# Performance work log

Measured on AMD Instinct MI355X. Metric: run time of the kernel, lower is better.

The kernel has to match this reference:

```python
import jax, jax.numpy as jnp
import numpy as np

B, T, F = 8, 512, 256
G, V = 2, 8192          # num_codebooks, num_embeddings per group
D = 16
DG = D // G             # per-group codevector dim = 8


def setup_inputs() -> dict:
    key = jax.random.key(0)
    k1, k2, k3, k4, k5 = jax.random.split(key, 5)
    x = jax.random.normal(k1, (B, T, F), dtype=jnp.float32)
    u = jax.random.uniform(k2, (B * T * G, V), dtype=jnp.float32)  # uniform for gumbel
    input_mask = jnp.ones((B, T), dtype=jnp.int32)
    embeddings = jax.random.uniform(k3, (1, G * V, DG), dtype=jnp.float32)
    W_proj = jax.random.normal(k4, (G * V, F), dtype=jnp.float32) * 0.02
    b_proj = jnp.zeros((G * V,), dtype=jnp.float32)
    return {"x": x, "u": u, "embeddings": embeddings,
            "W_proj": W_proj, "b_proj": b_proj, "input_mask": input_mask}


def reference(x, u, embeddings, W_proj, b_proj, input_mask):
    temperature = 1.0
    b, t, _ = x.shape
    # weight projection: [b, t, G*V]
    hidden = jnp.einsum("btf,gf->btg", x, W_proj) + b_proj
    h = hidden.reshape(b * t * G, V)
    # gumbel noise from uniform sample (matches torch.empty().uniform_(tiny, 1))
    tiny = jnp.finfo(h.dtype).tiny
    gumbels = -jnp.log(-jnp.log(jnp.clip(u, tiny, 1.0)))
    codevector_probs = jax.nn.softmax((h + gumbels) / temperature, axis=-1)  # [btG, V]
    # soft distribution (no noise) for perplexity
    soft = jax.nn.softmax(h.reshape(b * t, G, V), axis=-1)
    mask = input_mask.reshape(-1).astype(bool)  # [bt]
    masked = jnp.where(mask[:, None, None], soft, 0.0)
    marginal = masked.sum(0) / input_mask.sum().astype(soft.dtype)  # [G, V]
    perplexity = jnp.exp(-jnp.sum(marginal * jnp.log(marginal + 1e-7), axis=-1)).sum()
    targets_idx = jnp.argmax(codevector_probs, axis=-1).reshape(b, t, G)
    # per-group weighted codebook combination as GEMM (no huge broadcast intermediate)
    pg = codevector_probs.reshape(b * t, G, V)
    emb = embeddings.reshape(G, V, DG)
    codevectors = jnp.einsum("ngv,gvd->ngd", pg, emb).reshape(b, t, G * DG)
    return (codevectors, perplexity, targets_idx)
```

## Files before the change

### kernel.cpp

```cpp
#include <hip/hip_runtime.h>
#include <hip/hip_bf16.h>
#include <math.h>

#define Mrows 4096
#define Kdim  256
#define Ncols 16384
#define Vsz   8192

typedef __attribute__((ext_vector_type(8))) short bf16x8;
typedef __attribute__((ext_vector_type(4))) float f32x4;

__global__ __launch_bounds__(256) void split_bf16(const float* __restrict__ src,
                                                  __hip_bfloat16* __restrict__ hi,
                                                  __hip_bfloat16* __restrict__ lo) {
    const int i = blockIdx.x * 256 + threadIdx.x;
    const float v = src[i];
    const __hip_bfloat16 h = __float2bfloat16(v);
    const float hf = __bfloat162float(h);
    hi[i] = h;
    lo[i] = __float2bfloat16(v - hf);
}

__global__ __launch_bounds__(256) void gemm_mfma(const __hip_bfloat16* __restrict__ Ahi,
                                                 const __hip_bfloat16* __restrict__ Alo,
                                                 const __hip_bfloat16* __restrict__ Bhi,
                                                 const __hip_bfloat16* __restrict__ Blo,
                                                 const float* __restrict__ bias,
                                                 float* __restrict__ hid, int r0) {
    __shared__ unsigned short Ah[128 * 32], Al[128 * 32], Bh[128 * 32], Bl[128 * 32];
    const int tid = threadIdx.x;
    const int lane = tid & 63;
    const int wave = tid >> 6;
    const int bm = blockIdx.x * 128;
    const int bn = blockIdx.y * 128;
    const int wm = (wave & 1) * 64;
    const int wn = (wave >> 1) * 64;
    const int lm = lane & 15;
    const int kq = (lane >> 4) * 8;

    f32x4 acc[4][4];
#pragma unroll
    for (int i = 0; i < 4; ++i)
#pragma unroll
        for (int j = 0; j < 4; ++j) acc[i][j] = (f32x4){0.f, 0.f, 0.f, 0.f};

    for (int k0 = 0; k0 < Kdim; k0 += 32) {
        __syncthreads();
#pragma unroll
        for (int t = 0; t < 2; ++t) {
            const int c = tid + t * 256;
            const int row = c >> 2;
            const int ko = (c & 3) * 8;
            const size_t ga = (size_t)(r0 + bm + row) * Kdim + k0 + ko;
            const size_t gb = (size_t)(bn + row) * Kdim + k0 + ko;
            *(uint4*)&Ah[row * 32 + ko] = *(const uint4*)(Ahi + ga);
            *(uint4*)&Al[row * 32 + ko] = *(const uint4*)(Alo + ga);
            *(uint4*)&Bh[row * 32 + ko] = *(const uint4*)(Bhi + gb);
            *(uint4*)&Bl[row * 32 + ko] = *(const uint4*)(Blo + gb);
        }
        __syncthreads();

        bf16x8 ah[4], al[4], bh[4], bl[4];
#pragma unroll
        for (int i = 0; i < 4; ++i) {
            ah[i] = *(const bf16x8*)&Ah[(wm + i * 16 + lm) * 32 + kq];
            al[i] = *(const bf16x8*)&Al[(wm + i * 16 + lm) * 32 + kq];
            bh[i] = *(const bf16x8*)&Bh[(wn + i * 16 + lm) * 32 + kq];
            bl[i] = *(const bf16x8*)&Bl[(wn + i * 16 + lm) * 32 + kq];
        }
#pragma unroll
        for (int i = 0; i < 4; ++i)
#pragma unroll
            for (int j = 0; j < 4; ++j) {
                acc[i][j] = __builtin_amdgcn_mfma_f32_16x16x32_bf16(ah[i], bh[j], acc[i][j], 0, 0, 0);
                acc[i][j] = __builtin_amdgcn_mfma_f32_16x16x32_bf16(ah[i], bl[j], acc[i][j], 0, 0, 0);
                acc[i][j] = __builtin_amdgcn_mfma_f32_16x16x32_bf16(al[i], bh[j], acc[i][j], 0, 0, 0);
            }
    }

    const int rbase = (lane >> 4) * 4;
#pragma unroll
    for (int j = 0; j < 4; ++j) {
        const int n = bn + wn + j * 16 + lm;
        const float bj = bias[n];
#pragma unroll
        for (int i = 0; i < 4; ++i) {
            const int m0 = bm + wm + i * 16 + rbase;
#pragma unroll
            for (int r2 = 0; r2 < 4; ++r2)
                hid[(size_t)(m0 + r2) * Ncols + n] = acc[i][j][r2] + bj;
        }
    }
}

__global__ __launch_bounds__(256) void phase2(const float* __restrict__ hid,
                                              const float* __restrict__ u,
                                              const float* __restrict__ emb,
                                              const int* __restrict__ mask,
                                              float* __restrict__ marginal,
                                              float* __restrict__ out,
                                              int r0) {
    const int g = blockIdx.y;
    const int n0 = r0 + blockIdx.x * 8;
    const int tid = threadIdx.x;
    const int lane = tid & 63;
    const int wid = tid >> 6;

    __shared__ float marg_s[32 * 256];
    __shared__ float sv1[4]; __shared__ int si1[4]; __shared__ float sv2[4];
    __shared__ float ss1[4], ss2[4], scv[4][8];

#pragma unroll
    for (int i = 0; i < 32; ++i) marg_s[(i << 8) + tid] = 0.f;

    const float* embg = emb + (size_t)g * Vsz * 8;
    float lg[32];

    for (int r = 0; r < 8; ++r) {
        const int n = n0 + r;
        const float* hrow = hid + (size_t)(n - r0) * Ncols + (size_t)g * Vsz;
        const float* urow = u + ((size_t)n * 2 + g) * Vsz;

        float mx1 = -INFINITY, mx2 = -INFINITY;
        int amax = 0;
#pragma unroll
        for (int i = 0; i < 32; ++i) {
            const int v = (i << 8) + tid;
            const float hv = hrow[v];
            float uu = urow[v];
            uu = fminf(fmaxf(uu, 1.17549435e-38f), 1.0f);
            const float d = uu - 1.0f;
            float q = 1.0f / 9.0f;
            q = fmaf(q, d, -0.125f);
            q = fmaf(q, d, 1.0f / 7.0f);
            q = fmaf(q, d, -1.0f / 6.0f);
            q = fmaf(q, d, 0.2f);
            q = fmaf(q, d, -0.25f);
            q = fmaf(q, d, 1.0f / 3.0f);
            q = fmaf(q, d, -0.5f);
            q = fmaf(q, d, 1.0f);
            const float inner = (d > -0.2f) ? (-d) * q : -__logf(uu);
            const float l = hv - __logf(inner);
            lg[i] = l;
            if (l > mx1) { mx1 = l; amax = v; }
            mx2 = fmaxf(mx2, hv);
        }
        float v1 = mx1; int i1 = amax; float v2 = mx2;
#pragma unroll
        for (int off = 32; off > 0; off >>= 1) {
            const float ov = __shfl_down(v1, off);
            const int oi = __shfl_down(i1, off);
            if (ov > v1 || (ov == v1 && oi < i1)) { v1 = ov; i1 = oi; }
            v2 = fmaxf(v2, __shfl_down(v2, off));
        }
        if (lane == 0) { sv1[wid] = v1; si1[wid] = i1; sv2[wid] = v2; }
        __syncthreads();
        if (tid == 0) {
            float bv = sv1[0]; int bi = si1[0]; float b2 = sv2[0];
            for (int w2 = 1; w2 < 4; ++w2) {
                if (sv1[w2] > bv || (sv1[w2] == bv && si1[w2] < bi)) { bv = sv1[w2]; bi = si1[w2]; }
                b2 = fmaxf(b2, sv2[w2]);
            }
            sv1[0] = bv; si1[0] = bi; sv2[0] = b2;
        }
        __syncthreads();
        const float M1 = sv1[0];
        const float M2 = sv2[0];
        const int AMAX = si1[0];

        float s1 = 0.f, s2 = 0.f;
        float cv[8];
#pragma unroll
        for (int d2 = 0; d2 < 8; ++d2) cv[d2] = 0.f;
#pragma unroll
        for (int i = 0; i < 32; ++i) {
            const int v = (i << 8) + tid;
            const float p = __expf(lg[i] - M1);
            s1 += p;
            const float4 e0 = *(const float4*)(embg + (size_t)v * 8);
            const float4 e1 = *(const float4*)(embg + (size_t)v * 8 + 4);
            cv[0] = fmaf(p, e0.x, cv[0]); cv[1] = fmaf(p, e0.y, cv[1]);
            cv[2] = fmaf(p, e0.z, cv[2]); cv[3] = fmaf(p, e0.w, cv[3]);
            cv[4] = fmaf(p, e1.x, cv[4]); cv[5] = fmaf(p, e1.y, cv[5]);
            cv[6] = fmaf(p, e1.z, cv[6]); cv[7] = fmaf(p, e1.w, cv[7]);
            const float qq = __expf(hrow[v] - M2);
            s2 += qq;
            lg[i] = qq;
        }
#pragma unroll
        for (int off = 32; off > 0; off >>= 1) {
            s1 += __shfl_down(s1, off);
            s2 += __shfl_down(s2, off);
        }
#pragma unroll
        for (int d2 = 0; d2 < 8; ++d2)
#pragma unroll
            for (int off = 32; off > 0; off >>= 1) cv[d2] += __shfl_down(cv[d2], off);
        if (lane == 0) {
            ss1[wid] = s1; ss2[wid] = s2;
#pragma unroll
            for (int d2 = 0; d2 < 8; ++d2) scv[wid][d2] = cv[d2];
        }
        __syncthreads();
        if (tid == 0) {
            ss1[0] = ss1[0] + ss1[1] + ss1[2] + ss1[3];
            ss2[0] = ss2[0] + ss2[1] + ss2[2] + ss2[3];
        }
        __syncthreads();
        const float S1 = ss1[0];
        const float S2 = ss2[0];
        if (tid < 8) {
            const float c = scv[0][tid] + scv[1][tid] + scv[2][tid] + scv[3][tid];
            out[(size_t)n * 16 + g * 8 + tid] = c / S1;
        }
        if (tid == 8) out[65537 + (size_t)n * 2 + g] = (float)AMAX;

        if (mask[n] != 0) {
            const float invS2 = 1.0f / S2;
#pragma unroll
            for (int i = 0; i < 32; ++i)
                marg_s[(i << 8) + tid] = fmaf(lg[i], invS2, marg_s[(i << 8) + tid]);
        }
        __syncthreads();
    }
#pragma unroll
    for (int i = 0; i < 32; ++i)
        atomicAdd(&marginal[g * Vsz + (i << 8) + tid], marg_s[(i << 8) + tid]);
}

__global__ __launch_bounds__(256) void ppl_kernel(const float* __restrict__ marginal,
                                                  const int* __restrict__ mask,
                                                  float* __restrict__ out) {
    const int tid = threadIdx.x;
    const int lane = tid & 63;
    const int wid = tid >> 6;
    __shared__ float red[4];
    __shared__ int redi[4];

    int ms = 0;
    for (int i = tid; i < Mrows; i += 256) ms += mask[i];
#pragma unroll
    for (int off = 32; off > 0; off >>= 1) ms += __shfl_down(ms, off);
    if (lane == 0) redi[wid] = ms;
    __syncthreads();
    const float inv = 1.0f / (float)(redi[0] + redi[1] + redi[2] + redi[3]);

    float ppl = 0.f;
    for (int g = 0; g < 2; ++g) {
        float part = 0.f;
        for (int v = tid; v < Vsz; v += 256) {
            const float m = marginal[g * Vsz + v] * inv;
            part += m * logf(m + 1e-7f);
        }
#pragma unroll
        for (int off = 32; off > 0; off >>= 1) part += __shfl_down(part, off);
        __syncthreads();
        if (lane == 0) red[wid] = part;
        __syncthreads();
        if (tid == 0) ppl += __expf(-(red[0] + red[1] + red[2] + red[3]));
        __syncthreads();
    }
    if (tid == 0) out[65536] = ppl;
}

extern "C" void kernel_launch(void* const* d_in, const int* in_sizes, int n_in,
                              void* d_out, int out_size, void* d_ws, size_t ws_size,
                              hipStream_t stream) {
    const float* x    = (const float*)d_in[0];
    const float* u    = (const float*)d_in[1];
    const float* emb  = (const float*)d_in[2];
    const float* w    = (const float*)d_in[3];
    const float* bias = (const float*)d_in[4];
    const int*   mask = (const int*)d_in[5];
    float* out = (float*)d_out;

    char* base = (char*)d_ws;
    float* marginal = (float*)base;
    __hip_bfloat16* Ahi = (__hip_bfloat16*)(base + 65536);
    __hip_bfloat16* Alo = Ahi + 1048576;
    __hip_bfloat16* Bhi = Alo + 1048576;
    __hip_bfloat16* Blo = Bhi + 4194304;
    const size_t hid_off = 65536 + 4194304 + 16777216;
    float* hid = (float*)(base + hid_off);

    size_t cap_rows = (ws_size > hid_off) ? (ws_size - hid_off) / ((size_t)Ncols * 4) : 0;
    int cr = (cap_rows >= Mrows) ? Mrows : (int)((cap_rows / 128) * 128);
    if (cr < 128) cr = 128;

    hipMemsetAsync(marginal, 0, 65536, stream);
    split_bf16<<<4096, 256, 0, stream>>>(x, Ahi, Alo);
    split_bf16<<<16384, 256, 0, stream>>>(w, Bhi, Blo);

    for (int r0 = 0; r0 < Mrows; r0 += cr) {
        const int rows = (Mrows - r0 < cr) ? (Mrows - r0) : cr;
        dim3 gg(rows / 128, Ncols / 128);
        gemm_mfma<<<gg, 256, 0, stream>>>(Ahi, Alo, Bhi, Blo, bias, hid, r0);
        dim3 pg(rows / 8, 2);
        phase2<<<pg, 256, 0, stream>>>(hid, u, emb, mask, marginal, out, r0);
    }
    ppl_kernel<<<1, 256, 0, stream>>>(marginal, mask, out);
}
```

Before: 896.1 us.

## Use direct global-to-LDS loads in GEMM and widen phase2 to 512 threads

The GEMM tile loads now use global_load_lds, so data goes straight into shared memory instead of passing through registers first. In phase2 the block grows to 512 threads, each handling 16 elements per row through float4 vector loads of hid and u rather than 32 scalar loads. The trailing per-row __syncthreads is removed, and the marginal atomics are remapped to the new layout. Risks: the LDS layout in the GEMM must still match the c*8 indexing, and removing the barrier relies on each thread owning its own marg_s entries.

New measurement: 887.5 us. No clear change (-1.0%).

```diff
diff --git a/kernel.cpp b/kernel.cpp
--- a/kernel.cpp
+++ b/kernel.cpp
@@ -9,6 +9,10 @@
 
 typedef __attribute__((ext_vector_type(8))) short bf16x8;
 typedef __attribute__((ext_vector_type(4))) float f32x4;
+
+#define GLD16(ldsp, gp) __builtin_amdgcn_global_load_lds(                          \
+    (const __attribute__((address_space(1))) unsigned int*)(gp),                   \
+    (__attribute__((address_space(3))) unsigned int*)(ldsp), 16, 0, 0)
 
 __global__ __launch_bounds__(256) void split_bf16(const float* __restrict__ src,
                                                   __hip_bfloat16* __restrict__ hi,
@@ -53,10 +57,10 @@
             const int ko = (c & 3) * 8;
             const size_t ga = (size_t)(r0 + bm + row) * Kdim + k0 + ko;
             const size_t gb = (size_t)(bn + row) * Kdim + k0 + ko;
-            *(uint4*)&Ah[row * 32 + ko] = *(const uint4*)(Ahi + ga);
-            *(uint4*)&Al[row * 32 + ko] = *(const uint4*)(Alo + ga);
-            *(uint4*)&Bh[row * 32 + ko] = *(const uint4*)(Bhi + gb);
-            *(uint4*)&Bl[row * 32 + ko] = *(const uint4*)(Blo + gb);
+            GLD16(&Ah[c * 8], Ahi + ga);
+            GLD16(&Al[c * 8], Alo + ga);
+            GLD16(&Bh[c * 8], Bhi + gb);
+            GLD16(&Bl[c * 8], Blo + gb);
         }
         __syncthreads();
 
@@ -93,28 +97,28 @@
     }
 }
 
-__global__ __launch_bounds__(256) void phase2(const float* __restrict__ hid,
-                                              const float* __restrict__ u,
-                                              const float* __restrict__ emb,
-                                              const int* __restrict__ mask,
-                                              float* __restrict__ marginal,
-                                              float* __restrict__ out,
-                                              int r0) {
+__global__ __launch_bounds__(512, 4) void phase2(const float* __restrict__ hid,
+                                                 const float* __restrict__ u,
+                                                 const float* __restrict__ emb,
+                                                 const int* __restrict__ mask,
+                                                 float* __restrict__ marginal,
+                                                 float* __restrict__ out,
+                                                 int r0) {
     const int g = blockIdx.y;
     const int n0 = r0 + blockIdx.x * 8;
     const int tid = threadIdx.x;
     const int lane = tid & 63;
     const int wid = tid >> 6;
 
-    __shared__ float marg_s[32 * 256];
-    __shared__ float sv1[4]; __shared__ int si1[4]; __shared__ float sv2[4];
-    __shared__ float ss1[4], ss2[4], scv[4][8];
-
-#pragma unroll
-    for (int i = 0; i < 32; ++i) marg_s[(i << 8) + tid] = 0.f;
+    __shared__ float marg_s[16 * 512];
+    __shared__ float sv1[8]; __shared__ int si1[8]; __shared__ float sv2[8];
+    __shared__ float ss1[8], ss2[8], scv[8][8];
+
+#pragma unroll
+    for (int k = 0; k < 16; ++k) marg_s[(k << 9) + tid] = 0.f;
 
     const float* embg = emb + (size_t)g * Vsz * 8;
-    float lg[32];
+    float lg[16];
 
     for (int r = 0; r < 8; ++r) {
         const int n = n0 + r;
@@ -124,40 +128,45 @@
         float mx1 = -INFINITY, mx2 = -INFINITY;
         int amax = 0;
 #pragma unroll
-        for (int i = 0; i < 32; ++i) {
-            const int v = (i << 8) + tid;
-            const float hv = hrow[v];
-            float uu = urow[v];
-            uu = fminf(fmaxf(uu, 1.17549435e-38f), 1.0f);
-            const float d = uu - 1.0f;
-            float q = 1.0f / 9.0f;
-            q = fmaf(q, d, -0.125f);
-            q = fmaf(q, d, 1.0f / 7.0f);
-            q = fmaf(q, d, -1.0f / 6.0f);
-            q = fmaf(q, d, 0.2f);
-            q = fmaf(q, d, -0.25f);
-            q = fmaf(q, d, 1.0f / 3.0f);
-            q = fmaf(q, d, -0.5f);
-            q = fmaf(q, d, 1.0f);
-            const float inner = (d > -0.2f) ? (-d) * q : -__logf(uu);
-            const float l = hv - __logf(inner);
-            lg[i] = l;
-            if (l > mx1) { mx1 = l; amax = v; }
-            mx2 = fmaxf(mx2, hv);
-        }
-        float v1 = mx1; int i1 = amax; float v2 = mx2;
+        for (int i = 0; i < 4; ++i) {
+            const int vb = (i << 11) + (tid << 2);
+            const float4 hv4 = *(const float4*)(hrow + vb);
+            const float4 uu4 = *(const float4*)(urow + vb);
+#define GUM(j, hv, uraw) {                                                        \
+            float uu = fminf(fmaxf((uraw), 1.17549435e-38f), 1.0f);               \
+            const float d = uu - 1.0f;                                            \
+            float q = 1.0f / 9.0f;                                                \
+            q = fmaf(q, d, -0.125f);                                              \
+            q = fmaf(q, d, 1.0f / 7.0f);                                          \
+            q = fmaf(q, d, -1.0f / 6.0f);                                         \
+            q = fmaf(q, d, 0.2f);                                                 \
+            q = fmaf(q, d, -0.25f);                                               \
+            q = fmaf(q, d, 1.0f / 3.0f);                                          \
+            q = fmaf(q, d, -0.5f);                                                \
+            q = fmaf(q, d, 1.0f);                                                 \
+            const float inner = (d > -0.2f) ? (-d) * q : -__logf(uu);             \
+            const float l = (hv) - __logf(inner);                                 \
+            lg[(i << 2) + (j)] = l;                                               \
+            if (l > mx1) { mx1 = l; amax = vb + (j); }                            \
+            mx2 = fmaxf(mx2, (hv)); }
+            GUM(0, hv4.x, uu4.x)
+            GUM(1, hv4.y, uu4.y)
+            GUM(2, hv4.z, uu4.z)
+            GUM(3, hv4.w, uu4.w)
+#undef GUM
+        }
 #pragma unroll
         for (int off = 32; off > 0; off >>= 1) {
-            const float ov = __shfl_down(v1, off);
-            const int oi = __shfl_down(i1, off);
-            if (ov > v1 || (ov == v1 && oi < i1)) { v1 = ov; i1 = oi; }
-            v2 = fmaxf(v2, __shfl_down(v2, off));
-        }
-        if (lane == 0) { sv1[wid] = v1; si1[wid] = i1; sv2[wid] = v2; }
+            const float ov = __shfl_down(mx1, off);
+            const int oi = __shfl_down(amax, off);
+            if (ov > mx1 || (ov == mx1 && oi < amax)) { mx1 = ov; amax = oi; }
+            mx2 = fmaxf(mx2, __shfl_down(mx2, off));
+        }
+        if (lane == 0) { sv1[wid] = mx1; si1[wid] = amax; sv2[wid] = mx2; }
         __syncthreads();
         if (tid == 0) {
             float bv = sv1[0]; int bi = si1[0]; float b2 = sv2[0];
-            for (int w2 = 1; w2 < 4; ++w2) {
+            for (int w2 = 1; w2 < 8; ++w2) {
                 if (sv1[w2] > bv || (sv1[w2] == bv && si1[w2] < bi)) { bv = sv1[w2]; bi = si1[w2]; }
                 b2 = fmaxf(b2, sv2[w2]);
             }
@@ -173,19 +182,26 @@
 #pragma unroll
         for (int d2 = 0; d2 < 8; ++d2) cv[d2] = 0.f;
 #pragma unroll
-        for (int i = 0; i < 32; ++i) {
-            const int v = (i << 8) + tid;
-            const float p = __expf(lg[i] - M1);
-            s1 += p;
-            const float4 e0 = *(const float4*)(embg + (size_t)v * 8);
-            const float4 e1 = *(const float4*)(embg + (size_t)v * 8 + 4);
-            cv[0] = fmaf(p, e0.x, cv[0]); cv[1] = fmaf(p, e0.y, cv[1]);
-            cv[2] = fmaf(p, e0.z, cv[2]); cv[3] = fmaf(p, e0.w, cv[3]);
-            cv[4] = fmaf(p, e1.x, cv[4]); cv[5] = fmaf(p, e1.y, cv[5]);
-            cv[6] = fmaf(p, e1.z, cv[6]); cv[7] = fmaf(p, e1.w, cv[7]);
-            const float qq = __expf(hrow[v] - M2);
-            s2 += qq;
-            lg[i] = qq;
+        for (int i = 0; i < 4; ++i) {
+            const int vb = (i << 11) + (tid << 2);
+            const float4 hv4 = *(const float4*)(hrow + vb);
+#define PB(j, hv) {                                                               \
+            const float p = __expf(lg[(i << 2) + (j)] - M1);                      \
+            s1 += p;                                                              \
+            const float4 e0 = *(const float4*)(embg + (size_t)(vb + (j)) * 8);    \
+            const float4 e1 = *(const float4*)(embg + (size_t)(vb + (j)) * 8 + 4);\
+            cv[0] = fmaf(p, e0.x, cv[0]); cv[1] = fmaf(p, e0.y, cv[1]);           \
+            cv[2] = fmaf(p, e0.z, cv[2]); cv[3] = fmaf(p, e0.w, cv[3]);           \
+            cv[4] = fmaf(p, e1.x, cv[4]); cv[5] = fmaf(p, e1.y, cv[5]);           \
+            cv[6] = fmaf(p, e1.z, cv[6]); cv[7] = fmaf(p, e1.w, cv[7]);           \
+            const float qq = __expf((hv) - M2);                                   \
+            s2 += qq;                                                             \
+            lg[(i << 2) + (j)] = qq; }
+            PB(0, hv4.x)
+            PB(1, hv4.y)
+            PB(2, hv4.z)
+            PB(3, hv4.w)
+#undef PB
         }
 #pragma unroll
         for (int off = 32; off > 0; off >>= 1) {
@@ -203,14 +219,17 @@
         }
         __syncthreads();
         if (tid == 0) {
-            ss1[0] = ss1[0] + ss1[1] + ss1[2] + ss1[3];
-            ss2[0] = ss2[0] + ss2[1] + ss2[2] + ss2[3];
+            float a = 0.f, b = 0.f;
+            for (int w2 = 0; w2 < 8; ++w2) { a += ss1[w2]; b += ss2[w2]; }
+            ss1[0] = a; ss2[0] = b;
         }
         __syncthreads();
         const float S1 = ss1[0];
         const float S2 = ss2[0];
         if (tid < 8) {
-            const float c = scv[0][tid] + scv[1][tid] + scv[2][tid] + scv[3][tid];
+            float c = 0.f;
+#pragma unroll
+            for (int w2 = 0; w2 < 8; ++w2) c += scv[w2][tid];
             out[(size_t)n * 16 + g * 8 + tid] = c / S1;
         }
         if (tid == 8) out[65537 + (size_t)n * 2 + g] = (float)AMAX;
@@ -218,14 +237,14 @@
         if (mask[n] != 0) {
             const float invS2 = 1.0f / S2;
 #pragma unroll
-            for (int i = 0; i < 32; ++i)
-                marg_s[(i << 8) + tid] = fmaf(lg[i], invS2, marg_s[(i << 8) + tid]);
-        }
-        __syncthreads();
-    }
-#pragma unroll
-    for (int i = 0; i < 32; ++i)
-        atomicAdd(&marginal[g * Vsz + (i << 8) + tid], marg_s[(i << 8) + tid]);
+            for (int k = 0; k < 16; ++k)
+                marg_s[(k << 9) + tid] = fmaf(lg[k], invS2, marg_s[(k << 9) + tid]);
+        }
+    }
+#pragma unroll
+    for (int k = 0; k < 16; ++k)
+        atomicAdd(&marginal[g * Vsz + ((k >> 2) << 11) + (tid << 2) + (k & 3)],
+                  marg_s[(k << 9) + tid]);
 }
 
 __global__ __launch_bounds__(256) void ppl_kernel(const float* __restrict__ marginal,
@@ -296,7 +315,7 @@
         dim3 gg(rows / 128, Ncols / 128);
         gemm_mfma<<<gg, 256, 0, stream>>>(Ahi, Alo, Bhi, Blo, bias, hid, r0);
         dim3 pg(rows / 8, 2);
-        phase2<<<pg, 256, 0, stream>>>(hid, u, emb, mask, marginal, out, r0);
+        phase2<<<pg, 512, 0, stream>>>(hid, u, emb, mask, marginal, out, r0);
     }
     ppl_kernel<<<1, 256, 0, stream>>>(marginal, mask, out);
 }
```

## Use direct global-to-LDS loads in GEMM and register-resident marginals in phase2

Applied to the files above, without the earlier changes.

The GEMM now fills LDS with global_load_lds 16-byte transfers instead of staging through registers. It loads B fragments per column inside the MFMA loop and requests 3 blocks per CU. Phase2 moves to 512-thread blocks, keeps the marginal accumulators and hidden values in registers instead of a 32KB LDS array, and drops a re-read of hid. The row chunk size is capped at 2048 so the hidden buffer stays smaller and more cache-friendly, at the cost of one extra launch pair.

Result: slower. 1.010 ms (+12.8%).

```diff
diff --git a/kernel.cpp b/kernel.cpp
--- a/kernel.cpp
+++ b/kernel.cpp
@@ -9,6 +9,10 @@
 
 typedef __attribute__((ext_vector_type(8))) short bf16x8;
 typedef __attribute__((ext_vector_type(4))) float f32x4;
+
+#define GLD16(ldsp, gp) __builtin_amdgcn_global_load_lds(                          \
+    (const __attribute__((address_space(1))) unsigned int*)(gp),                   \
+    (__attribute__((address_space(3))) unsigned int*)(ldsp), 16, 0, 0)
 
 __global__ __launch_bounds__(256) void split_bf16(const float* __restrict__ src,
                                                   __hip_bfloat16* __restrict__ hi,
@@ -21,12 +25,12 @@
     lo[i] = __float2bfloat16(v - hf);
 }
 
-__global__ __launch_bounds__(256) void gemm_mfma(const __hip_bfloat16* __restrict__ Ahi,
-                                                 const __hip_bfloat16* __restrict__ Alo,
-                                                 const __hip_bfloat16* __restrict__ Bhi,
-                                                 const __hip_bfloat16* __restrict__ Blo,
-                                                 const float* __restrict__ bias,
-                                                 float* __restrict__ hid, int r0) {
+__global__ __launch_bounds__(256, 3) void gemm_mfma(const __hip_bfloat16* __restrict__ Ahi,
+                                                    const __hip_bfloat16* __restrict__ Alo,
+                                                    const __hip_bfloat16* __restrict__ Bhi,
+                                                    const __hip_bfloat16* __restrict__ Blo,
+                                                    const float* __restrict__ bias,
+                                                    float* __restrict__ hid, int r0) {
     __shared__ unsigned short Ah[128 * 32], Al[128 * 32], Bh[128 * 32], Bl[128 * 32];
     const int tid = threadIdx.x;
     const int lane = tid & 63;
@@ -53,29 +57,30 @@
             const int ko = (c & 3) * 8;
             const size_t ga = (size_t)(r0 + bm + row) * Kdim + k0 + ko;
             const size_t gb = (size_t)(bn + row) * Kdim + k0 + ko;
-            *(uint4*)&Ah[row * 32 + ko] = *(const uint4*)(Ahi + ga);
-            *(uint4*)&Al[row * 32 + ko] = *(const uint4*)(Alo + ga);
-            *(uint4*)&Bh[row * 32 + ko] = *(const uint4*)(Bhi + gb);
-            *(uint4*)&Bl[row * 32 + ko] = *(const uint4*)(Blo + gb);
-        }
-        __syncthreads();
-
-        bf16x8 ah[4], al[4], bh[4], bl[4];
+            GLD16(&Ah[c * 8], Ahi + ga);
+            GLD16(&Al[c * 8], Alo + ga);
+            GLD16(&Bh[c * 8], Bhi + gb);
+            GLD16(&Bl[c * 8], Blo + gb);
+        }
+        __syncthreads();
+
+        bf16x8 ah[4], al[4];
 #pragma unroll
         for (int i = 0; i < 4; ++i) {
             ah[i] = *(const bf16x8*)&Ah[(wm + i * 16 + lm) * 32 + kq];
             al[i] = *(const bf16x8*)&Al[(wm + i * 16 + lm) * 32 + kq];
-            bh[i] = *(const bf16x8*)&Bh[(wn + i * 16 + lm) * 32 + kq];
-            bl[i] = *(const bf16x8*)&Bl[(wn + i * 16 + lm) * 32 + kq];
-        }
-#pragma unroll
-        for (int i = 0; i < 4; ++i)
-#pragma unroll
-            for (int j = 0; j < 4; ++j) {
-                acc[i][j] = __builtin_amdgcn_mfma_f32_16x16x32_bf16(ah[i], bh[j], acc[i][j], 0, 0, 0);
-                acc[i][j] = __builtin_amdgcn_mfma_f32_16x16x32_bf16(ah[i], bl[j], acc[i][j], 0, 0, 0);
-                acc[i][j] = __builtin_amdgcn_mfma_f32_16x16x32_bf16(al[i], bh[j], acc[i][j], 0, 0, 0);
+        }
+#pragma unroll
+        for (int j = 0; j < 4; ++j) {
+            const bf16x8 bh = *(const bf16x8*)&Bh[(wn + j * 16 + lm) * 32 + kq];
+            const bf16x8 bl = *(const bf16x8*)&Bl[(wn + j * 16 + lm) * 32 + kq];
+#pragma unroll
+            for (int i = 0; i < 4; ++i) {
+                acc[i][j] = __builtin_amdgcn_mfma_f32_16x16x32_bf16(ah[i], bh, acc[i][j], 0, 0, 0);
+                acc[i][j] = __builtin_amdgcn_mfma_f32_16x16x32_bf16(ah[i], bl, acc[i][j], 0, 0, 0);
+                acc[i][j] = __builtin_amdgcn_mfma_f32_16x16x32_bf16(al[i], bh, acc[i][j], 0, 0, 0);
             }
+        }
     }
 
     const int rbase = (lane >> 4) * 4;
@@ -93,28 +98,27 @@
     }
 }
 
-__global__ __launch_bounds__(256) void phase2(const float* __restrict__ hid,
-                                              const float* __restrict__ u,
-                                              const float* __restrict__ emb,
-                                              const int* __restrict__ mask,
-                                              float* __restrict__ marginal,
-                                              float* __restrict__ out,
-                                              int r0) {
+__global__ __launch_bounds__(512, 4) void phase2(const float* __restrict__ hid,
+                                                 const float* __restrict__ u,
+                                                 const float* __restrict__ emb,
+                                                 const int* __restrict__ mask,
+                                                 float* __restrict__ marginal,
+                                                 float* __restrict__ out,
+                                                 int r0) {
     const int g = blockIdx.y;
     const int n0 = r0 + blockIdx.x * 8;
     const int tid = threadIdx.x;
     const int lane = tid & 63;
     const int wid = tid >> 6;
 
-    __shared__ float marg_s[32 * 256];
-    __shared__ float sv1[4]; __shared__ int si1[4]; __shared__ float sv2[4];
-    __shared__ float ss1[4], ss2[4], scv[4][8];
-
-#pragma unroll
-    for (int i = 0; i < 32; ++i) marg_s[(i << 8) + tid] = 0.f;
+    __shared__ float sv1[8]; __shared__ int si1[8]; __shared__ float sv2[8];
+    __shared__ float ss1[8], ss2[8], scv[8][8];
 
     const float* embg = emb + (size_t)g * Vsz * 8;
-    float lg[32];
+    float marg[16];
+#pragma unroll
+    for (int k = 0; k < 16; ++k) marg[k] = 0.f;
+    float lg[16], hv[16];
 
     for (int r = 0; r < 8; ++r) {
         const int n = n0 + r;
@@ -124,11 +128,11 @@
         float mx1 = -INFINITY, mx2 = -INFINITY;
         int amax = 0;
 #pragma unroll
-        for (int i = 0; i < 32; ++i) {
-            const int v = (i << 8) + tid;
-            const float hv = hrow[v];
-            float uu = urow[v];
-            uu = fminf(fmaxf(uu, 1.17549435e-38f), 1.0f);
+        for (int k = 0; k < 16; ++k) {
+            const int v = (k << 9) + tid;
+            const float h = hrow[v];
+            const float uraw = urow[v];
+            float uu = fminf(fmaxf(uraw, 1.17549435e-38f), 1.0f);
             const float d = uu - 1.0f;
             float q = 1.0f / 9.0f;
             q = fmaf(q, d, -0.125f);
@@ -140,24 +144,24 @@
             q = fmaf(q, d, -0.5f);
             q = fmaf(q, d, 1.0f);
             const float inner = (d > -0.2f) ? (-d) * q : -__logf(uu);
-            const float l = hv - __logf(inner);
-            lg[i] = l;
+            const float l = h - __logf(inner);
+            lg[k] = l;
+            hv[k] = h;
             if (l > mx1) { mx1 = l; amax = v; }
-            mx2 = fmaxf(mx2, hv);
-        }
-        float v1 = mx1; int i1 = amax; float v2 = mx2;
+            mx2 = fmaxf(mx2, h);
+        }
 #pragma unroll
         for (int off = 32; off > 0; off >>= 1) {
-            const float ov = __shfl_down(v1, off);
-            const int oi = __shfl_down(i1, off);
-            if (ov > v1 || (ov == v1 && oi < i1)) { v1 = ov; i1 = oi; }
-            v2 = fmaxf(v2, __shfl_down(v2, off));
-        }
-        if (lane == 0) { sv1[wid] = v1; si1[wid] = i1; sv2[wid] = v2; }
+            const float ov = __shfl_down(mx1, off);
+            const int oi = __shfl_down(amax, off);
+            if (ov > mx1 || (ov == mx1 && oi < amax)) { mx1 = ov; amax = oi; }
+            mx2 = fmaxf(mx2, __shfl_down(mx2, off));
+        }
+        if (lane == 0) { sv1[wid] = mx1; si1[wid] = amax; sv2[wid] = mx2; }
         __syncthreads();
         if (tid == 0) {
             float bv = sv1[0]; int bi = si1[0]; float b2 = sv2[0];
-            for (int w2 = 1; w2 < 4; ++w2) {
+            for (int w2 = 1; w2 < 8; ++w2) {
                 if (sv1[w2] > bv || (sv1[w2] == bv && si1[w2] < bi)) { bv = sv1[w2]; bi = si1[w2]; }
                 b2 = fmaxf(b2, sv2[w2]);
             }
@@ -173,9 +177,9 @@
 #pragma unroll
         for (int d2 = 0; d2 < 8; ++d2) cv[d2] = 0.f;
 #pragma unroll
-        for (int i = 0; i < 32; ++i) {
-            const int v = (i << 8) + tid;
-            const float p = __expf(lg[i] - M1);
+        for (int k = 0; k < 16; ++k) {
+            const int v = (k << 9) + tid;
+            const float p = __expf(lg[k] - M1);
             s1 += p;
             const float4 e0 = *(const float4*)(embg + (size_t)v * 8);
             const float4 e1 = *(const float4*)(embg + (size_t)v * 8 + 4);
@@ -183,9 +187,9 @@
             cv[2] = fmaf(p, e0.z, cv[2]); cv[3] = fmaf(p, e0.w, cv[3]);
             cv[4] = fmaf(p, e1.x, cv[4]); cv[5] = fmaf(p, e1.y, cv[5]);
             cv[6] = fmaf(p, e1.z, cv[6]); cv[7] = fmaf(p, e1.w, cv[7]);
-            const float qq = __expf(hrow[v] - M2);
+            const float qq = __expf(hv[k] - M2);
             s2 += qq;
-            lg[i] = qq;
+            lg[k] = qq;
         }
 #pragma unroll
         for (int off = 32; off > 0; off >>= 1) {
@@ -203,14 +207,17 @@
         }
         __syncthreads();
         if (tid == 0) {
-            ss1[0] = ss1[0] + ss1[1] + ss1[2] + ss1[3];
-            ss2[0] = ss2[0] + ss2[1] + ss2[2] + ss2[3];
+            float a = 0.f, b = 0.f;
+            for (int w2 = 0; w2 < 8; ++w2) { a += ss1[w2]; b += ss2[w2]; }
+            ss1[0] = a; ss2[0] = b;
         }
         __syncthreads();
         const float S1 = ss1[0];
         const float S2 = ss2[0];
         if (tid < 8) {
-            const float c = scv[0][tid] + scv[1][tid] + scv[2][tid] + scv[3][tid];
+            float c = 0.f;
+#pragma unroll
+            for (int w2 = 0; w2 < 8; ++w2) c += scv[w2][tid];
             out[(size_t)n * 16 + g * 8 + tid] = c / S1;
         }
         if (tid == 8) out[65537 + (size_t)n * 2 + g] = (float)AMAX;
@@ -218,14 +225,13 @@
         if (mask[n] != 0) {
             const float invS2 = 1.0f / S2;
 #pragma unroll
-            for (int i = 0; i < 32; ++i)
-                marg_s[(i << 8) + tid] = fmaf(lg[i], invS2, marg_s[(i << 8) + tid]);
-        }
-        __syncthreads();
-    }
-#pragma unroll
-    for (int i = 0; i < 32; ++i)
-        atomicAdd(&marginal[g * Vsz + (i << 8) + tid], marg_s[(i << 8) + tid]);
+            for (int k = 0; k < 16; ++k)
+                marg[k] = fmaf(lg[k], invS2, marg[k]);
+        }
+    }
+#pragma unroll
+    for (int k = 0; k < 16; ++k)
+        atomicAdd(&marginal[g * Vsz + (k << 9) + tid], marg[k]);
 }
 
 __global__ __launch_bounds__(256) void ppl_kernel(const float* __restrict__ marginal,
@@ -286,6 +292,7 @@
     size_t cap_rows = (ws_size > hid_off) ? (ws_size - hid_off) / ((size_t)Ncols * 4) : 0;
     int cr = (cap_rows >= Mrows) ? Mrows : (int)((cap_rows / 128) * 128);
     if (cr < 128) cr = 128;
+    if (cr > 2048) cr = 2048;
 
     hipMemsetAsync(marginal, 0, 65536, stream);
     split_bf16<<<4096, 256, 0, stream>>>(x, Ahi, Alo);
@@ -296,7 +303,7 @@
         dim3 gg(rows / 128, Ncols / 128);
         gemm_mfma<<<gg, 256, 0, stream>>>(Ahi, Alo, Bhi, Blo, bias, hid, r0);
         dim3 pg(rows / 8, 2);
-        phase2<<<pg, 256, 0, stream>>>(hid, u, emb, mask, marginal, out, r0);
+        phase2<<<pg, 512, 0, stream>>>(hid, u, emb, mask, marginal, out, r0);
     }
     ppl_kernel<<<1, 256, 0, stream>>>(marginal, mask, out);
 }
```
